# Optimization experiments

Measured on AMD Instinct MI355X. Metric: run time of the kernel, lower is better.

The kernel has to match this reference:

```python
import jax, jax.numpy as jnp
import numpy as np

N_VOX = 400000
C = 64
BATCH, T, H, W = 2, 21, 400, 400


def _layernorm(x, g, b, eps=1e-5):
    m = x.mean(-1, keepdims=True)
    v = ((x - m) ** 2).mean(-1, keepdims=True)
    return (x - m) * jax.lax.rsqrt(v + eps) * g + b


def _subm_conv3(feats, coords, lin, w, t_dim, h_dim, w_dim):
    # Submanifold 3x3x3 conv: output defined only at active sites; for each of the
    # 27 offsets, look up the neighbor via binary search on the sorted linear index.
    st = h_dim * w_dim
    sh = w_dim
    n = feats.shape[0]
    out = jnp.zeros((n, w.shape[-1]), feats.dtype)
    for kt in range(3):
        for ky in range(3):
            for kx in range(3):
                dt, dy, dx = kt - 1, ky - 1, kx - 1
                tt = coords[:, 1] + dt
                yy = coords[:, 2] + dy
                xx = coords[:, 3] + dx
                valid = (tt >= 0) & (tt < t_dim) & (yy >= 0) & (yy < h_dim) & (xx >= 0) & (xx < w_dim)
                nb = lin + dt * st + dy * sh + dx
                pos = jnp.clip(jnp.searchsorted(lin, nb), 0, n - 1)
                found = valid & (lin[pos] == nb)
                nb_f = jnp.where(found[:, None], feats[pos], jnp.zeros((), feats.dtype))
                out = out + nb_f @ w[kt, ky, kx]
    return out


def setup_inputs() -> dict:
    key = jax.random.key(0)
    ks = jax.random.split(key, 8)
    rng = np.random.default_rng(0)
    total = BATCH * T * H * W
    lin_np = np.sort(rng.choice(total, N_VOX, replace=False)).astype(np.int64)
    b = lin_np // (T * H * W)
    r = lin_np % (T * H * W)
    t = r // (H * W)
    r = r % (H * W)
    y = r // W
    x = r % W
    indices = jnp.asarray(np.stack([b, t, y, x], axis=1).astype(np.int32))
    features = jax.random.normal(ks[0], (N_VOX, C), dtype=jnp.float32)
    conv1_w = jax.random.normal(ks[1], (3, 3, 3, C, C), dtype=jnp.float32) * 0.05
    conv2_w = jax.random.normal(ks[2], (3, 3, 3, C, C), dtype=jnp.float32) * 0.05
    ln1_g = jnp.ones((C,), jnp.float32)
    ln1_b = jnp.zeros((C,), jnp.float32)
    ln2_g = jnp.ones((C,), jnp.float32)
    ln2_b = jnp.zeros((C,), jnp.float32)
    return {"features": features, "indices": indices, "conv1_w": conv1_w,
            "ln1_g": ln1_g, "ln1_b": ln1_b, "conv2_w": conv2_w,
            "ln2_g": ln2_g, "ln2_b": ln2_b,
            "spatial_T": T, "spatial_H": H, "spatial_W": W}


def reference(features, indices, conv1_w, ln1_g, ln1_b, conv2_w, ln2_g, ln2_b,
              spatial_T, spatial_H, spatial_W):
    coords = indices.astype(jnp.int64)
    st_b = spatial_T * spatial_H * spatial_W
    lin = (coords[:, 0] * st_b + coords[:, 1] * (spatial_H * spatial_W)
           + coords[:, 2] * spatial_W + coords[:, 3])  # sorted ascending by construction
    # conv1 -> LN -> ReLU
    out = _subm_conv3(features, coords, lin, conv1_w, spatial_T, spatial_H, spatial_W)
    out = jax.nn.relu(_layernorm(out, ln1_g, ln1_b))
    # conv2 -> LN (stride=1 path: submanifold conv, same index set)
    out = _subm_conv3(out, coords, lin, conv2_w, spatial_T, spatial_H, spatial_W)
    out = _layernorm(out, ln2_g, ln2_b)
    # sparse_add: both tensors share the identical sorted index set, so the
    # scatter-add over unique linear indices reduces to elementwise add
    # (zero-feature pruning omitted: probability ~0 with continuous data).
    out = out + features
    return jax.nn.relu(out)
```

## Files before the change

### kernel.cpp

```cpp
#include <hip/hip_runtime.h>


#define SBB_T 21
#define SBB_H 400
#define SBB_W 400
#define SBB_TOTAL (2 * SBB_T * SBB_H * SBB_W)

__global__ void sbb_lin_kernel(const int* idxs, int* lin, int n) {
    int i = blockIdx.x * 256 + threadIdx.x;
    if (i < n) {
        int b = idxs[4 * i];
        int t = idxs[4 * i + 1];
        int y = idxs[4 * i + 2];
        int x = idxs[4 * i + 3];
        lin[i] = ((b * 21 + t) * 400 + y) * 400 + x;
    }
}

__global__ void sbb_map_init(int* map) {
    int i = blockIdx.x * 256 + threadIdx.x;
    if (i < SBB_TOTAL) map[i] = -1;
}

__global__ void sbb_map_set(const int* lin, int* map, int n) {
    int i = blockIdx.x * 256 + threadIdx.x;
    if (i < n) map[lin[i]] = i;
}

__global__ void sbb_fill_kernel(float* p, int nel, float val) {
    int i = blockIdx.x * 256 + threadIdx.x;
    if (i < nel) p[i] = val;
}

__device__ __forceinline__ float sbb_bf2f(unsigned short u) {
    return __uint_as_float(((unsigned)u) << 16);
}

__global__ void SparseBasicBlock_69965017252009_kernel(
    const float* featsf,
    const unsigned short* featsb,
    const float* w,
    const float* gamma,
    const float* beta,
    const float* residual,
    float* outf,
    unsigned short* outb,
    const int* lin,
    const int* idxs,
    const int* map,
    int n,
    int use_residual,
    int feats_bf16,
    int out_bf16,
    int use_map)
{
    int tid = threadIdx.x;
    int vox = blockIdx.x * 4 + (tid >> 6);
    if (vox >= n) return;
    int co = tid & 63;

    int t0 = idxs[4 * vox + 1];
    int y0 = idxs[4 * vox + 2];
    int x0 = idxs[4 * vox + 3];
    int mylin = lin[vox];

    float acc = 0.0f;

    #pragma unroll
    for (int dt = -1; dt <= 1; ++dt) {
        int tt = t0 + dt;
        if (tt < 0 || tt >= SBB_T) continue;
        #pragma unroll
        for (int dy = -1; dy <= 1; ++dy) {
            int yy = y0 + dy;
            if (yy < 0 || yy >= SBB_H) continue;
            #pragma unroll
            for (int dx = -1; dx <= 1; ++dx) {
                int xx = x0 + dx;
                if (xx < 0 || xx >= SBB_W) continue;

                int key = mylin + dt * (SBB_H * SBB_W) + dy * SBB_W + dx;
                int lo;
                if (use_map) {
                    lo = map[key];
                } else {
                    int l = 0, h = n;
                    while (l < h) {
                        int m = (l + h) >> 1;
                        if (lin[m] < key) l = m + 1; else h = m;
                    }
                    lo = (l < n && lin[l] == key) ? l : -1;
                }
                if (lo < 0) continue;

                int kk = (dt + 1) * 9 + (dy + 1) * 3 + (dx + 1);
                const float* wr = w + kk * 4096 + co;
                if (feats_bf16) {
                    const unsigned short* fr = featsb + (size_t)lo * 64;
                    #pragma unroll 4
                    for (int c4 = 0; c4 < 16; ++c4) {
                        ushort4 fv = *(const ushort4*)(fr + c4 * 4);
                        const float* wp = wr + c4 * 256;
                        acc += sbb_bf2f(fv.x) * wp[0];
                        acc += sbb_bf2f(fv.y) * wp[64];
                        acc += sbb_bf2f(fv.z) * wp[128];
                        acc += sbb_bf2f(fv.w) * wp[192];
                    }
                } else {
                    const float4* fr = (const float4*)(featsf + (size_t)lo * 64);
                    #pragma unroll 4
                    for (int c4 = 0; c4 < 16; ++c4) {
                        float4 fv = fr[c4];
                        const float* wp = wr + c4 * 256;
                        acc += fv.x * wp[0];
                        acc += fv.y * wp[64];
                        acc += fv.z * wp[128];
                        acc += fv.w * wp[192];
                    }
                }
            }
        }
    }

    float s = acc, q = acc * acc;
    #pragma unroll
    for (int m = 32; m > 0; m >>= 1) {
        s += __shfl_xor(s, m, 64);
        q += __shfl_xor(q, m, 64);
    }
    float mean = s * 0.015625f;
    float var = q * 0.015625f - mean * mean;
    if (var < 0.0f) var = 0.0f;
    float rstd = rsqrtf(var + 1e-5f);

    float yv = (acc - mean) * rstd * gamma[co] + beta[co];
    int oi = vox * 64 + co;
    if (use_residual) yv += residual[oi];
    if (yv < 0.0f) yv = 0.0f;
    if (out_bf16) {
        unsigned u = __float_as_uint(yv);
        unsigned r = u + 0x7fffu + ((u >> 16) & 1u);
        outb[oi] = (unsigned short)(r >> 16);
    } else {
        outf[oi] = yv;
    }
}

extern "C" void kernel_launch(void* const* d_in, const int* in_sizes, int n_in,
                              void* d_out, int out_size, void* d_ws, size_t ws_size,
                              hipStream_t stream) {
    const float* feats = (const float*)d_in[0];
    const int* idxs = (const int*)d_in[1];
    const float* w1 = (const float*)d_in[2];
    const float* g1 = (const float*)d_in[3];
    const float* b1 = (const float*)d_in[4];
    const float* w2 = (const float*)d_in[5];
    const float* g2 = (const float*)d_in[6];
    const float* b2 = (const float*)d_in[7];
    float* out = (float*)d_out;

    int n = 400000;

    size_t lin_b = (size_t)n * 4;
    size_t map_b = (size_t)SBB_TOTAL * 4;
    size_t mid_b = (size_t)n * 128;
    size_t need_min  = lin_b + mid_b;
    size_t need_full = lin_b + map_b + mid_b;

    if (ws_size < need_min) {
        sbb_fill_kernel<<<(n * 64 + 255) / 256, 256, 0, stream>>>(out, n * 64, 1000.0f);
        return;
    }

    int* lin = (int*)d_ws;
    int use_map = (ws_size >= need_full) ? 1 : 0;
    int* map = nullptr;
    unsigned short* mid;
    if (use_map) {
        map = (int*)((char*)d_ws + lin_b);
        mid = (unsigned short*)((char*)d_ws + lin_b + map_b);
    } else {
        mid = (unsigned short*)((char*)d_ws + lin_b);
    }

    sbb_lin_kernel<<<(n + 255) / 256, 256, 0, stream>>>(idxs, lin, n);
    if (use_map) {
        sbb_map_init<<<(SBB_TOTAL + 255) / 256, 256, 0, stream>>>(map);
        sbb_map_set<<<(n + 255) / 256, 256, 0, stream>>>(lin, map, n);
    }

    SparseBasicBlock_69965017252009_kernel<<<n / 4, 256, 0, stream>>>(
        feats, (const unsigned short*)feats, w1, g1, b1, feats,
        (float*)mid, mid, lin, idxs, map, n, 0, 0, 1, use_map);

    SparseBasicBlock_69965017252009_kernel<<<n / 4, 256, 0, stream>>>(
        feats, mid, w2, g2, b2, feats,
        out, (unsigned short*)out, lin, idxs, map, n, 1, 1, 0, use_map);
}
```

Before: 2.145 ms.

## Tile conv over 128 voxels per block with shared-memory weights and neighbor table

New measurement: 2.200 ms. +2.5%, slower.

```diff
diff --git a/kernel.cpp b/kernel.cpp
--- a/kernel.cpp
+++ b/kernel.cpp
@@ -5,6 +5,12 @@
 #define SBB_H 400
 #define SBB_W 400
 #define SBB_TOTAL (2 * SBB_T * SBB_H * SBB_W)
+#define SBB_N 400000
+
+#define WT_STRIDE 68
+#define WT_TILE (64 * WT_STRIDE)
+#define VPB 128
+#define VPW 32
 
 __global__ void sbb_lin_kernel(const int* idxs, int* lin, int n) {
     int i = blockIdx.x * 256 + threadIdx.x;
@@ -27,31 +33,206 @@
     if (i < n) map[lin[i]] = i;
 }
 
+__global__ void sbb_wt_kernel(const float* __restrict__ w, float* __restrict__ wt) {
+    int k = blockIdx.x;
+    const float* ws = w + (size_t)k * 4096;
+    float* wd = wt + (size_t)k * WT_TILE;
+    for (int e = threadIdx.x; e < 4096; e += 256) {
+        int ci = e >> 6;
+        int co = e & 63;
+        wd[co * WT_STRIDE + ci] = ws[e];
+    }
+}
+
 __global__ void sbb_fill_kernel(float* p, int nel, float val) {
     int i = blockIdx.x * 256 + threadIdx.x;
     if (i < nel) p[i] = val;
 }
 
-__device__ __forceinline__ float sbb_bf2f(unsigned short u) {
-    return __uint_as_float(((unsigned)u) << 16);
-}
-
-__global__ void SparseBasicBlock_69965017252009_kernel(
-    const float* featsf,
-    const unsigned short* featsb,
-    const float* w,
-    const float* gamma,
-    const float* beta,
-    const float* residual,
-    float* outf,
-    unsigned short* outb,
-    const int* lin,
-    const int* idxs,
-    const int* map,
-    int n,
-    int use_residual,
-    int feats_bf16,
-    int out_bf16,
+template<int IN_BF16, int OUT_BF16, int USE_RES>
+__global__ __launch_bounds__(256, 3)
+void sbb_conv(
+    const float* __restrict__ featsf,
+    const unsigned short* __restrict__ featsb,
+    const float* __restrict__ wt,
+    const float* __restrict__ gamma,
+    const float* __restrict__ beta,
+    const float* __restrict__ residual,
+    float* __restrict__ outf,
+    unsigned short* __restrict__ outb,
+    const int* __restrict__ lin,
+    const int* __restrict__ idxs,
+    const int* __restrict__ map,
+    int n)
+{
+    __shared__ int s_lin[VPB];
+    __shared__ int s_tyx[VPB];
+    __shared__ int s_nbr[27 * VPB];
+    __shared__ __align__(16) float s_w[2][WT_TILE];
+
+    int tid = threadIdx.x;
+    int vox0 = blockIdx.x * VPB;
+
+    if (tid < VPB) {
+        int v = vox0 + tid;
+        if (v < n) {
+            const int4 q = *(const int4*)(idxs + 4 * (size_t)v);
+            s_tyx[tid] = (q.y << 20) | (q.z << 10) | q.w;
+            s_lin[tid] = lin[v];
+        } else {
+            s_tyx[tid] = 0;
+            s_lin[tid] = -1;
+        }
+    }
+    __syncthreads();
+
+    #pragma unroll 4
+    for (int j = tid; j < 27 * VPB; j += 256) {
+        int k = j >> 7;
+        int v = j & (VPB - 1);
+        int dt = k / 9 - 1;
+        int rem = k % 9;
+        int dy = rem / 3 - 1;
+        int dx = rem % 3 - 1;
+        int tyx = s_tyx[v];
+        int t0 = tyx >> 20, y0 = (tyx >> 10) & 1023, x0 = tyx & 1023;
+        int ml = s_lin[v];
+        int tt = t0 + dt, yy = y0 + dy, xx = x0 + dx;
+        bool valid = (ml >= 0) & ((unsigned)tt < 21u) & ((unsigned)yy < 400u)
+                   & ((unsigned)xx < 400u);
+        int key = ml + dt * (SBB_H * SBB_W) + dy * SBB_W + dx;
+        int ck = valid ? key : 0;
+        int lo = map[ck];
+        s_nbr[j] = valid ? lo : -1;
+    }
+
+    {
+        const float* src = wt;
+        #pragma unroll
+        for (int c = 0; c < 4; ++c) {
+            int idx = tid + c * 256;
+            uint4 d = *(const uint4*)(src + (size_t)idx * 4);
+            *(uint4*)&s_w[0][idx * 4] = d;
+        }
+        if (tid < 64) {
+            int idx = tid + 1024;
+            uint4 d = *(const uint4*)(src + (size_t)idx * 4);
+            *(uint4*)&s_w[0][idx * 4] = d;
+        }
+    }
+
+    int wid = tid >> 6;
+    int co = tid & 63;
+    int vbase = wid * VPW;
+
+    float acc[VPW];
+    #pragma unroll
+    for (int v = 0; v < VPW; ++v) acc[v] = 0.0f;
+
+    for (int k = 0; k < 27; ++k) {
+        __syncthreads();
+        int cur = k & 1;
+
+        uint4 r0, r1, r2, r3, r4;
+        if (k < 26) {
+            const float* src = wt + (size_t)(k + 1) * WT_TILE;
+            r0 = *(const uint4*)(src + (size_t)(tid + 0) * 4);
+            r1 = *(const uint4*)(src + (size_t)(tid + 256) * 4);
+            r2 = *(const uint4*)(src + (size_t)(tid + 512) * 4);
+            r3 = *(const uint4*)(src + (size_t)(tid + 768) * 4);
+            if (tid < 64) r4 = *(const uint4*)(src + (size_t)(tid + 1024) * 4);
+        }
+
+        float4 w4[16];
+        #pragma unroll
+        for (int j = 0; j < 16; ++j)
+            w4[j] = *(const float4*)&s_w[cur][co * WT_STRIDE + j * 4];
+
+        const int* nb = &s_nbr[(k << 7) + vbase];
+        #pragma unroll
+        for (int v4 = 0; v4 < VPW / 4; ++v4) {
+            int4 nq = *(const int4*)(nb + v4 * 4);
+            #pragma unroll
+            for (int u = 0; u < 4; ++u) {
+                int lo = (u == 0) ? nq.x : (u == 1) ? nq.y : (u == 2) ? nq.z : nq.w;
+                if (lo < 0) continue;
+                const int vv = v4 * 4 + u;
+                if (IN_BF16) {
+                    const uint4* fb = (const uint4*)(featsb + (size_t)lo * 64);
+                    #pragma unroll
+                    for (int j2 = 0; j2 < 8; ++j2) {
+                        uint4 uu = fb[j2];
+                        float4 wa = w4[2 * j2], wb = w4[2 * j2 + 1];
+                        acc[vv] += __uint_as_float(uu.x << 16) * wa.x;
+                        acc[vv] += __uint_as_float(uu.x & 0xffff0000u) * wa.y;
+                        acc[vv] += __uint_as_float(uu.y << 16) * wa.z;
+                        acc[vv] += __uint_as_float(uu.y & 0xffff0000u) * wa.w;
+                        acc[vv] += __uint_as_float(uu.z << 16) * wb.x;
+                        acc[vv] += __uint_as_float(uu.z & 0xffff0000u) * wb.y;
+                        acc[vv] += __uint_as_float(uu.w << 16) * wb.z;
+                        acc[vv] += __uint_as_float(uu.w & 0xffff0000u) * wb.w;
+                    }
+                } else {
+                    const float4* fr = (const float4*)(featsf + (size_t)lo * 64);
+                    #pragma unroll
+                    for (int j = 0; j < 16; ++j) {
+                        float4 f = fr[j];
+                        float4 ww = w4[j];
+                        acc[vv] += f.x * ww.x;
+                        acc[vv] += f.y * ww.y;
+                        acc[vv] += f.z * ww.z;
+                        acc[vv] += f.w * ww.w;
+                    }
+                }
+            }
+        }
+
+        if (k < 26) {
+            int nxt = cur ^ 1;
+            *(uint4*)&s_w[nxt][(tid + 0) * 4] = r0;
+            *(uint4*)&s_w[nxt][(tid + 256) * 4] = r1;
+            *(uint4*)&s_w[nxt][(tid + 512) * 4] = r2;
+            *(uint4*)&s_w[nxt][(tid + 768) * 4] = r3;
+            if (tid < 64) *(uint4*)&s_w[nxt][(tid + 1024) * 4] = r4;
+        }
+    }
+
+    float g = gamma[co], b = beta[co];
+    #pragma unroll
+    for (int v = 0; v < VPW; ++v) {
+        int vx = vox0 + vbase + v;
+        float a = acc[v];
+        float s = a, q = a * a;
+        #pragma unroll
+        for (int m = 32; m > 0; m >>= 1) {
+            s += __shfl_xor(s, m, 64);
+            q += __shfl_xor(q, m, 64);
+        }
+        float mean = s * 0.015625f;
+        float var = q * 0.015625f - mean * mean;
+        var = var < 0.0f ? 0.0f : var;
+        float rstd = rsqrtf(var + 1e-5f);
+        float yv = (a - mean) * rstd * g + b;
+        if (vx < n) {
+            size_t oi = (size_t)vx * 64 + co;
+            if (USE_RES) yv += residual[oi];
+            if (yv < 0.0f) yv = 0.0f;
+            if (OUT_BF16) {
+                unsigned uu = __float_as_uint(yv);
+                unsigned rr = uu + 0x7fffu + ((uu >> 16) & 1u);
+                outb[oi] = (unsigned short)(rr >> 16);
+            } else {
+                outf[oi] = yv;
+            }
+        }
+    }
+}
+
+__global__ void sbb_conv_old(
+    const float* featsf, const unsigned short* featsb, const float* w,
+    const float* gamma, const float* beta, const float* residual,
+    float* outf, unsigned short* outb, const int* lin, const int* idxs,
+    const int* map, int n, int use_residual, int feats_bf16, int out_bf16,
     int use_map)
 {
     int tid = threadIdx.x;
@@ -65,7 +246,6 @@
     int mylin = lin[vox];
 
     float acc = 0.0f;
-
     #pragma unroll
     for (int dt = -1; dt <= 1; ++dt) {
         int tt = t0 + dt;
@@ -78,7 +258,6 @@
             for (int dx = -1; dx <= 1; ++dx) {
                 int xx = x0 + dx;
                 if (xx < 0 || xx >= SBB_W) continue;
-
                 int key = mylin + dt * (SBB_H * SBB_W) + dy * SBB_W + dx;
                 int lo;
                 if (use_map) {
@@ -92,7 +271,6 @@
                     lo = (l < n && lin[l] == key) ? l : -1;
                 }
                 if (lo < 0) continue;
-
                 int kk = (dt + 1) * 9 + (dy + 1) * 3 + (dx + 1);
                 const float* wr = w + kk * 4096 + co;
                 if (feats_bf16) {
@@ -101,10 +279,10 @@
                     for (int c4 = 0; c4 < 16; ++c4) {
                         ushort4 fv = *(const ushort4*)(fr + c4 * 4);
                         const float* wp = wr + c4 * 256;
-                        acc += sbb_bf2f(fv.x) * wp[0];
-                        acc += sbb_bf2f(fv.y) * wp[64];
-                        acc += sbb_bf2f(fv.z) * wp[128];
-                        acc += sbb_bf2f(fv.w) * wp[192];
+                        acc += __uint_as_float(((unsigned)fv.x) << 16) * wp[0];
+                        acc += __uint_as_float(((unsigned)fv.y) << 16) * wp[64];
+                        acc += __uint_as_float(((unsigned)fv.z) << 16) * wp[128];
+                        acc += __uint_as_float(((unsigned)fv.w) << 16) * wp[192];
                     }
                 } else {
                     const float4* fr = (const float4*)(featsf + (size_t)lo * 64);
@@ -159,13 +337,18 @@
     const float* b2 = (const float*)d_in[7];
     float* out = (float*)d_out;
 
-    int n = 400000;
+    int n = SBB_N;
 
     size_t lin_b = (size_t)n * 4;
     size_t map_b = (size_t)SBB_TOTAL * 4;
-    size_t mid_b = (size_t)n * 128;
-    size_t need_min  = lin_b + mid_b;
-    size_t need_full = lin_b + map_b + mid_b;
+    size_t wt_b  = (size_t)27 * WT_TILE * 4;
+    size_t midf_b = (size_t)n * 64 * 4;
+    size_t midb_b = (size_t)n * 64 * 2;
+
+    size_t need_T2  = lin_b + map_b + 2 * wt_b + midf_b;
+    size_t need_T1  = lin_b + map_b + 2 * wt_b + midb_b;
+    size_t need_old = lin_b + map_b + midb_b;
+    size_t need_min = lin_b + midb_b;
 
     if (ws_size < need_min) {
         sbb_fill_kernel<<<(n * 64 + 255) / 256, 256, 0, stream>>>(out, n * 64, 1000.0f);
@@ -173,7 +356,43 @@
     }
 
     int* lin = (int*)d_ws;
-    int use_map = (ws_size >= need_full) ? 1 : 0;
+    int grid_lin = (n + 255) / 256;
+
+    if (ws_size >= need_T1) {
+        int* map = (int*)((char*)d_ws + lin_b);
+        float* wt1 = (float*)((char*)d_ws + lin_b + map_b);
+        float* wt2 = wt1 + (size_t)27 * WT_TILE;
+        char* midp = (char*)d_ws + lin_b + map_b + 2 * wt_b;
+        int mid_f32 = (ws_size >= need_T2) ? 1 : 0;
+
+        sbb_lin_kernel<<<grid_lin, 256, 0, stream>>>(idxs, lin, n);
+        sbb_map_init<<<(SBB_TOTAL + 255) / 256, 256, 0, stream>>>(map);
+        sbb_map_set<<<grid_lin, 256, 0, stream>>>(lin, map, n);
+        sbb_wt_kernel<<<27, 256, 0, stream>>>(w1, wt1);
+        sbb_wt_kernel<<<27, 256, 0, stream>>>(w2, wt2);
+
+        int grid_conv = (n + VPB - 1) / VPB;
+        if (mid_f32) {
+            float* mid = (float*)midp;
+            sbb_conv<0, 0, 0><<<grid_conv, 256, 0, stream>>>(
+                feats, (const unsigned short*)feats, wt1, g1, b1, feats,
+                mid, (unsigned short*)mid, lin, idxs, map, n);
+            sbb_conv<0, 0, 1><<<grid_conv, 256, 0, stream>>>(
+                mid, (const unsigned short*)mid, wt2, g2, b2, feats,
+                out, (unsigned short*)out, lin, idxs, map, n);
+        } else {
+            unsigned short* mid = (unsigned short*)midp;
+            sbb_conv<0, 1, 0><<<grid_conv, 256, 0, stream>>>(
+                feats, (const unsigned short*)feats, wt1, g1, b1, feats,
+                (float*)mid, mid, lin, idxs, map, n);
+            sbb_conv<1, 0, 1><<<grid_conv, 256, 0, stream>>>(
+                feats, mid, wt2, g2, b2, feats,
+                out, (unsigned short*)out, lin, idxs, map, n);
+        }
+        return;
+    }
+
+    int use_map = (ws_size >= need_old) ? 1 : 0;
     int* map = nullptr;
     unsigned short* mid;
     if (use_map) {
@@ -183,17 +402,16 @@
         mid = (unsigned short*)((char*)d_ws + lin_b);
     }
 
-    sbb_lin_kernel<<<(n + 255) / 256, 256, 0, stream>>>(idxs, lin, n);
+    sbb_lin_kernel<<<grid_lin, 256, 0, stream>>>(idxs, lin, n);
     if (use_map) {
         sbb_map_init<<<(SBB_TOTAL + 255) / 256, 256, 0, stream>>>(map);
-        sbb_map_set<<<(n + 255) / 256, 256, 0, stream>>>(lin, map, n);
-    }
-
-    SparseBasicBlock_69965017252009_kernel<<<n / 4, 256, 0, stream>>>(
+        sbb_map_set<<<grid_lin, 256, 0, stream>>>(lin, map, n);
+    }
+
+    sbb_conv_old<<<n / 4, 256, 0, stream>>>(
         feats, (const unsigned short*)feats, w1, g1, b1, feats,
         (float*)mid, mid, lin, idxs, map, n, 0, 0, 1, use_map);
-
-    SparseBasicBlock_69965017252009_kernel<<<n / 4, 256, 0, stream>>>(
+    sbb_conv_old<<<n / 4, 256, 0, stream>>>(
         feats, mid, w2, g2, b2, feats,
         out, (unsigned short*)out, lin, idxs, map, n, 1, 1, 0, use_map);
 }
```

## Add blocked sparse conv kernel with shared neighbor table and transposed weights

Applied to the files above, without the earlier changes.

Result: slower. 2.582 ms (+20.4%).

```diff
diff --git a/kernel.cpp b/kernel.cpp
--- a/kernel.cpp
+++ b/kernel.cpp
@@ -5,6 +5,13 @@
 #define SBB_H 400
 #define SBB_W 400
 #define SBB_TOTAL (2 * SBB_T * SBB_H * SBB_W)
+#define SBB_N 400000
+
+__device__ __forceinline__ unsigned short sbb_f2b(float f) {
+    unsigned u = __float_as_uint(f);
+    unsigned r = u + 0x7fffu + ((u >> 16) & 1u);
+    return (unsigned short)(r >> 16);
+}
 
 __global__ void sbb_lin_kernel(const int* idxs, int* lin, int n) {
     int i = blockIdx.x * 256 + threadIdx.x;
@@ -22,36 +29,161 @@
     if (i < SBB_TOTAL) map[i] = -1;
 }
 
+__global__ void sbb_map_set2(const int* __restrict__ idxs, int* __restrict__ map, int n) {
+    int i = blockIdx.x * 256 + threadIdx.x;
+    if (i < n) {
+        int4 q = ((const int4*)idxs)[i];
+        int li = ((q.x * 21 + q.y) * 400 + q.z) * 400 + q.w;
+        map[li] = i;
+    }
+}
+
 __global__ void sbb_map_set(const int* lin, int* map, int n) {
     int i = blockIdx.x * 256 + threadIdx.x;
     if (i < n) map[lin[i]] = i;
 }
 
+__global__ void sbb_wt2(const float* __restrict__ w, float* __restrict__ wt) {
+    int k = blockIdx.x;
+    const float* ws = w + (size_t)k * 4096;
+    float* wd = wt + (size_t)k * 4096;
+    for (int e = threadIdx.x; e < 4096; e += 256) {
+        int ci = e >> 6;
+        int co = e & 63;
+        wd[co * 64 + ci] = ws[e];
+    }
+}
+
 __global__ void sbb_fill_kernel(float* p, int nel, float val) {
     int i = blockIdx.x * 256 + threadIdx.x;
     if (i < nel) p[i] = val;
 }
 
-__device__ __forceinline__ float sbb_bf2f(unsigned short u) {
-    return __uint_as_float(((unsigned)u) << 16);
-}
-
-__global__ void SparseBasicBlock_69965017252009_kernel(
-    const float* featsf,
-    const unsigned short* featsb,
-    const float* w,
-    const float* gamma,
-    const float* beta,
-    const float* residual,
-    float* outf,
-    unsigned short* outb,
-    const int* lin,
-    const int* idxs,
-    const int* map,
-    int n,
-    int use_residual,
-    int feats_bf16,
-    int out_bf16,
+template<int USE_RES>
+__global__ __launch_bounds__(256)
+void sbb_conv4(const float* __restrict__ A,
+               const float* __restrict__ wt,
+               const float* __restrict__ gamma,
+               const float* __restrict__ beta,
+               const float* __restrict__ residual,
+               float* __restrict__ out,
+               const int* __restrict__ idxs,
+               const int* __restrict__ map,
+               const float* __restrict__ zpage,
+               int n)
+{
+    __shared__ int s_nbr[27 * 16];
+    __shared__ int s_lin[16];
+    __shared__ int s_tyx[16];
+
+    int tid = threadIdx.x;
+    int lane = tid & 63;
+    int wid = tid >> 6;
+    int co = lane;
+    int vox0 = blockIdx.x * 16;
+
+    if (tid < 16) {
+        int v = vox0 + tid;
+        int4 q = *(const int4*)(idxs + 4 * (size_t)v);
+        s_tyx[tid] = (q.y << 20) | (q.z << 10) | q.w;
+        s_lin[tid] = ((q.x * 21 + q.y) * 400 + q.z) * 400 + q.w;
+    }
+    __syncthreads();
+
+    for (int j = tid; j < 27 * 16; j += 256) {
+        int k = j >> 4;
+        int v = j & 15;
+        int dt = k / 9 - 1;
+        int rem = k % 9;
+        int dy = rem / 3 - 1;
+        int dx = rem % 3 - 1;
+        int tyx = s_tyx[v];
+        int t0 = tyx >> 20, y0 = (tyx >> 10) & 1023, x0 = tyx & 1023;
+        int tt = t0 + dt, yy = y0 + dy, xx = x0 + dx;
+        bool valid = ((unsigned)tt < 21u) & ((unsigned)yy < 400u)
+                   & ((unsigned)xx < 400u);
+        int key = s_lin[v] + dt * (SBB_H * SBB_W) + dy * SBB_W + dx;
+        int lo = map[valid ? key : 0];
+        s_nbr[j] = valid ? lo : -1;
+    }
+    __syncthreads();
+
+    float acc0 = 0.f, acc1 = 0.f, acc2 = 0.f, acc3 = 0.f;
+    int vb = wid * 4;
+
+    for (int k = 0; k < 27; ++k) {
+        int nb0 = s_nbr[(k << 4) + vb + 0];
+        int nb1 = s_nbr[(k << 4) + vb + 1];
+        int nb2 = s_nbr[(k << 4) + vb + 2];
+        int nb3 = s_nbr[(k << 4) + vb + 3];
+        int mx01 = nb0 > nb1 ? nb0 : nb1;
+        int mx23 = nb2 > nb3 ? nb2 : nb3;
+        if ((mx01 > mx23 ? mx01 : mx23) < 0) continue;
+
+        nb0 = __builtin_amdgcn_readfirstlane(nb0);
+        nb1 = __builtin_amdgcn_readfirstlane(nb1);
+        nb2 = __builtin_amdgcn_readfirstlane(nb2);
+        nb3 = __builtin_amdgcn_readfirstlane(nb3);
+        const float* b0 = (nb0 >= 0) ? A + (size_t)nb0 * 64 : zpage;
+        const float* b1 = (nb1 >= 0) ? A + (size_t)nb1 * 64 : zpage;
+        const float* b2 = (nb2 >= 0) ? A + (size_t)nb2 * 64 : zpage;
+        const float* b3 = (nb3 >= 0) ? A + (size_t)nb3 * 64 : zpage;
+
+        const float* wr = wt + ((size_t)k << 12) + (co << 6);
+
+        #pragma unroll
+        for (int c4 = 0; c4 < 16; ++c4) {
+            float4 w4 = *(const float4*)(wr + c4 * 4);
+            float4 f0 = *(const float4*)(b0 + c4 * 4);
+            float4 f1 = *(const float4*)(b1 + c4 * 4);
+            float4 f2 = *(const float4*)(b2 + c4 * 4);
+            float4 f3 = *(const float4*)(b3 + c4 * 4);
+            acc0 = fmaf(f0.x, w4.x, acc0);
+            acc0 = fmaf(f0.y, w4.y, acc0);
+            acc0 = fmaf(f0.z, w4.z, acc0);
+            acc0 = fmaf(f0.w, w4.w, acc0);
+            acc1 = fmaf(f1.x, w4.x, acc1);
+            acc1 = fmaf(f1.y, w4.y, acc1);
+            acc1 = fmaf(f1.z, w4.z, acc1);
+            acc1 = fmaf(f1.w, w4.w, acc1);
+            acc2 = fmaf(f2.x, w4.x, acc2);
+            acc2 = fmaf(f2.y, w4.y, acc2);
+            acc2 = fmaf(f2.z, w4.z, acc2);
+            acc2 = fmaf(f2.w, w4.w, acc2);
+            acc3 = fmaf(f3.x, w4.x, acc3);
+            acc3 = fmaf(f3.y, w4.y, acc3);
+            acc3 = fmaf(f3.z, w4.z, acc3);
+            acc3 = fmaf(f3.w, w4.w, acc3);
+        }
+    }
+
+    float g = gamma[co], bv = beta[co];
+    #pragma unroll
+    for (int v = 0; v < 4; ++v) {
+        float a = (v == 0) ? acc0 : (v == 1) ? acc1 : (v == 2) ? acc2 : acc3;
+        float s = a, q = a * a;
+        #pragma unroll
+        for (int msk = 32; msk > 0; msk >>= 1) {
+            s += __shfl_xor(s, msk, 64);
+            q += __shfl_xor(q, msk, 64);
+        }
+        float mean = s * 0.015625f;
+        float var = q * 0.015625f - mean * mean;
+        var = var < 0.f ? 0.f : var;
+        float rstd = rsqrtf(var + 1e-5f);
+        float y = (a - mean) * rstd * g + bv;
+        size_t oi = (size_t)(vox0 + vb + v) * 64 + co;
+        if (USE_RES) y += residual[oi];
+        if (y < 0.f) y = 0.f;
+        out[oi] = y;
+    }
+}
+
+__global__ void sbb_conv_old(
+    const float* featsf, const unsigned short* featsb, const float* w,
+    const float* gamma, const float* beta, const float* residual,
+    float* outf, unsigned short* outb, const int* lin, const int* idxs,
+    const int* map, int n, int use_residual, int feats_bf16, int out_bf16,
     int use_map)
 {
     int tid = threadIdx.x;
@@ -65,7 +197,6 @@
     int mylin = lin[vox];
 
     float acc = 0.0f;
-
     #pragma unroll
     for (int dt = -1; dt <= 1; ++dt) {
         int tt = t0 + dt;
@@ -78,7 +209,6 @@
             for (int dx = -1; dx <= 1; ++dx) {
                 int xx = x0 + dx;
                 if (xx < 0 || xx >= SBB_W) continue;
-
                 int key = mylin + dt * (SBB_H * SBB_W) + dy * SBB_W + dx;
                 int lo;
                 if (use_map) {
@@ -86,13 +216,12 @@
                 } else {
                     int l = 0, h = n;
                     while (l < h) {
-                        int m = (l + h) >> 1;
-                        if (lin[m] < key) l = m + 1; else h = m;
+                        int mm = (l + h) >> 1;
+                        if (lin[mm] < key) l = mm + 1; else h = mm;
                     }
                     lo = (l < n && lin[l] == key) ? l : -1;
                 }
                 if (lo < 0) continue;
-
                 int kk = (dt + 1) * 9 + (dy + 1) * 3 + (dx + 1);
                 const float* wr = w + kk * 4096 + co;
                 if (feats_bf16) {
@@ -101,10 +230,10 @@
                     for (int c4 = 0; c4 < 16; ++c4) {
                         ushort4 fv = *(const ushort4*)(fr + c4 * 4);
                         const float* wp = wr + c4 * 256;
-                        acc += sbb_bf2f(fv.x) * wp[0];
-                        acc += sbb_bf2f(fv.y) * wp[64];
-                        acc += sbb_bf2f(fv.z) * wp[128];
-                        acc += sbb_bf2f(fv.w) * wp[192];
+                        acc += __uint_as_float(((unsigned)fv.x) << 16) * wp[0];
+                        acc += __uint_as_float(((unsigned)fv.y) << 16) * wp[64];
+                        acc += __uint_as_float(((unsigned)fv.z) << 16) * wp[128];
+                        acc += __uint_as_float(((unsigned)fv.w) << 16) * wp[192];
                     }
                 } else {
                     const float4* fr = (const float4*)(featsf + (size_t)lo * 64);
@@ -124,9 +253,9 @@
 
     float s = acc, q = acc * acc;
     #pragma unroll
-    for (int m = 32; m > 0; m >>= 1) {
-        s += __shfl_xor(s, m, 64);
-        q += __shfl_xor(q, m, 64);
+    for (int mm = 32; mm > 0; mm >>= 1) {
+        s += __shfl_xor(s, mm, 64);
+        q += __shfl_xor(q, mm, 64);
     }
     float mean = s * 0.015625f;
     float var = q * 0.015625f - mean * mean;
@@ -138,9 +267,7 @@
     if (use_residual) yv += residual[oi];
     if (yv < 0.0f) yv = 0.0f;
     if (out_bf16) {
-        unsigned u = __float_as_uint(yv);
-        unsigned r = u + 0x7fffu + ((u >> 16) & 1u);
-        outb[oi] = (unsigned short)(r >> 16);
+        outb[oi] = sbb_f2b(yv);
     } else {
         outf[oi] = yv;
     }
@@ -159,21 +286,48 @@
     const float* b2 = (const float*)d_in[7];
     float* out = (float*)d_out;
 
-    int n = 400000;
-
-    size_t lin_b = (size_t)n * 4;
-    size_t map_b = (size_t)SBB_TOTAL * 4;
-    size_t mid_b = (size_t)n * 128;
-    size_t need_min  = lin_b + mid_b;
-    size_t need_full = lin_b + map_b + mid_b;
+    int n = SBB_N;
+
+    size_t map_b  = (size_t)SBB_TOTAL * 4;
+    size_t midf_b = (size_t)n * 64 * 4;
+    size_t wt_b   = (size_t)27 * 4096 * 4;
+    size_t zb_b   = 512;
+    size_t lin_b  = (size_t)n * 4;
+    size_t midb_b = (size_t)n * 64 * 2;
+
+    size_t need_new = map_b + midf_b + 2 * wt_b + zb_b;
+    size_t need_old = lin_b + map_b + midb_b;
+    size_t need_min = lin_b + midb_b;
+
+    if (ws_size >= need_new) {
+        char* p = (char*)d_ws;
+        int* map = (int*)p;          p += map_b;
+        float* mid = (float*)p;      p += midf_b;
+        float* wt1 = (float*)p;      p += wt_b;
+        float* wt2 = (float*)p;      p += wt_b;
+        float* zb = (float*)p;
+
+        sbb_map_init<<<(SBB_TOTAL + 255) / 256, 256, 0, stream>>>(map);
+        sbb_map_set2<<<(n + 255) / 256, 256, 0, stream>>>(idxs, map, n);
+        sbb_wt2<<<27, 256, 0, stream>>>(w1, wt1);
+        sbb_wt2<<<27, 256, 0, stream>>>(w2, wt2);
+        sbb_fill_kernel<<<1, 256, 0, stream>>>(zb, 128, 0.0f);
+
+        int grid_conv = n / 16;
+        sbb_conv4<0><<<grid_conv, 256, 0, stream>>>(
+            feats, wt1, g1, b1, feats, mid, idxs, map, zb, n);
+        sbb_conv4<1><<<grid_conv, 256, 0, stream>>>(
+            mid, wt2, g2, b2, feats, out, idxs, map, zb, n);
+        return;
+    }
 
     if (ws_size < need_min) {
         sbb_fill_kernel<<<(n * 64 + 255) / 256, 256, 0, stream>>>(out, n * 64, 1000.0f);
         return;
     }
 
+    int use_map = (ws_size >= need_old) ? 1 : 0;
     int* lin = (int*)d_ws;
-    int use_map = (ws_size >= need_full) ? 1 : 0;
     int* map = nullptr;
     unsigned short* mid;
     if (use_map) {
@@ -183,17 +337,17 @@
         mid = (unsigned short*)((char*)d_ws + lin_b);
     }
 
-    sbb_lin_kernel<<<(n + 255) / 256, 256, 0, stream>>>(idxs, lin, n);
+    int grid_lin = (n + 255) / 256;
+    sbb_lin_kernel<<<grid_lin, 256, 0, stream>>>(idxs, lin, n);
     if (use_map) {
         sbb_map_init<<<(SBB_TOTAL + 255) / 256, 256, 0, stream>>>(map);
-        sbb_map_set<<<(n + 255) / 256, 256, 0, stream>>>(lin, map, n);
-    }
-
-    SparseBasicBlock_69965017252009_kernel<<<n / 4, 256, 0, stream>>>(
+        sbb_map_set<<<grid_lin, 256, 0, stream>>>(lin, map, n);
+    }
+
+    sbb_conv_old<<<n / 4, 256, 0, stream>>>(
         feats, (const unsigned short*)feats, w1, g1, b1, feats,
         (float*)mid, mid, lin, idxs, map, n, 0, 0, 1, use_map);
-
-    SparseBasicBlock_69965017252009_kernel<<<n / 4, 256, 0, stream>>>(
+    sbb_conv_old<<<n / 4, 256, 0, stream>>>(
         feats, mid, w2, g2, b2, feats,
         out, (unsigned short*)out, lin, idxs, map, n, 1, 1, 0, use_map);
 }
```
